# Kernel optimization log

Measured on AMD Instinct MI355X. Metric: run time of the kernel, lower is better.

Reference implementation:

```python
import jax, jax.numpy as jnp
import numpy as np

NUM_HEADS = 8


def setup_inputs() -> dict:
    key = jax.random.key(0)
    ks = jax.random.split(key, 10)
    B, C, H, W = 8, 256, 128, 128
    x_c = jax.random.normal(ks[0], (B, C, H, W), dtype=jnp.float32)
    x_t = jax.random.normal(ks[1], (B, C, H, W), dtype=jnp.float32)
    std = 0.02
    Wq = jax.random.normal(ks[2], (C, C), dtype=jnp.float32) * std
    Wk = jax.random.normal(ks[3], (C, C), dtype=jnp.float32) * std
    Wv = jax.random.normal(ks[4], (C, C), dtype=jnp.float32) * std
    Wo = jax.random.normal(ks[5], (C, C), dtype=jnp.float32) * std
    bq = jnp.zeros((C,), jnp.float32)
    bk = jnp.zeros((C,), jnp.float32)
    bv = jnp.zeros((C,), jnp.float32)
    bo = jnp.zeros((C,), jnp.float32)
    return {"x_c": x_c, "x_t": x_t, "Wq": Wq, "bq": bq, "Wk": Wk, "bk": bk,
            "Wv": Wv, "bv": bv, "Wo": Wo, "bo": bo}


def reference(x_c, x_t, Wq, bq, Wk, bk, Wv, bv, Wo, bo):
    B, C, H, W = x_c.shape
    nh = NUM_HEADS
    hd = C // nh                       # head_dim = in_chans // num_heads
    scale = hd ** (-0.5)
    N = H * W

    # fuse_type == 'add'
    x = (x_c + x_t).transpose(0, 2, 3, 1)          # [B,H,W,C]

    # torch Linear: y = x @ W.T + b
    q = x @ Wq.T + bq
    k = x @ Wk.T + bk
    v = x @ Wv.T + bv

    # 'b h w (c head) -> b (h w) head c' : head is the INNER split factor
    def split_heads(t):
        return t.reshape(B, N, hd, nh).transpose(0, 1, 3, 2)  # [B,N,nh,hd]

    q, k, v = split_heads(q), split_heads(k), split_heads(v)

    # attention ACROSS heads per token: [B,N,nh,nh] (faithful to source)
    dot = jnp.einsum('bnhc,bngc->bnhg', q, k) * scale
    attn = jax.nn.softmax(dot, axis=-1)
    o = jnp.einsum('bnhg,bngc->bnhc', attn, v)     # [B,N,nh,hd]

    # 'b (h w) head c -> b h w (head c)' : head is the OUTER concat factor
    o = o.reshape(B, H, W, nh * hd)
    out = o @ Wo.T + bo                            # [B,H,W,C]
    return out.transpose(0, 3, 1, 2)               # [B,C,H,W]
```

## Files before the change

### kernel.cpp

```cpp
#include <hip/hip_runtime.h>
#include <hip/hip_bf16.h>


typedef unsigned short u16;
typedef __bf16 bf16x8 __attribute__((ext_vector_type(8)));
typedef float f32x4 __attribute__((ext_vector_type(4)));
typedef unsigned short u16x8 __attribute__((ext_vector_type(8)));
typedef unsigned short u16x4 __attribute__((ext_vector_type(4)));

constexpr int CH = 256;
constexpr int HWN = 16384;
constexpr int LDX = 264;
constexpr int LQ = 776;

constexpr size_t WS_WQKV = 0;
constexpr size_t WS_WO = 393216;
constexpr size_t WS_BIAS = 524288;
constexpr size_t WS_O = 528384;

__device__ __forceinline__ u16 f2bf(float f) {
    unsigned u = __builtin_bit_cast(unsigned, f);
    unsigned r = u + 0x7FFFu + ((u >> 16) & 1u);
    return (u16)(r >> 16);
}
__device__ __forceinline__ float bf2f(u16 u) {
    return __builtin_bit_cast(float, (unsigned)u << 16);
}

__global__ void prep_kernel(const float* __restrict__ Wq, const float* __restrict__ Wk,
                            const float* __restrict__ Wv, const float* __restrict__ Wo,
                            const float* __restrict__ bq, const float* __restrict__ bk,
                            const float* __restrict__ bv,
                            u16* __restrict__ Wqkv_b, u16* __restrict__ Wo_b,
                            float* __restrict__ bias_qkv) {
    const int i = blockIdx.x;
    const int c = threadIdx.x;
    const int j = i & 255;
    const int p = ((j & 31) << 3) + (j >> 5);
    const float* Wsrc = (i < 256) ? Wq : (i < 512 ? Wk : Wv);
    const float* bsrc = (i < 256) ? bq : (i < 512 ? bk : bv);
    Wqkv_b[i * 256 + c] = f2bf(Wsrc[p * 256 + c]);
    if (i < 256) Wo_b[i * 256 + c] = f2bf(Wo[i * 256 + c]);
    if (c == 0) bias_qkv[i] = bsrc[p];
}

__launch_bounds__(512, 2)
__global__ void qkv_attn_kernel(const float* __restrict__ x_c, const float* __restrict__ x_t,
                                const u16* __restrict__ Wqkv_b,
                                const float* __restrict__ bias_qkv,
                                u16* __restrict__ O_glob) {
    __shared__ u16 XT[64 * LDX];
    __shared__ u16 QKVT[64 * LQ];

    const int tid = threadIdx.x;
    const int lane = tid & 63;
    const int wave = tid >> 6;
    const long tok0 = (long)blockIdx.x * 64;
    const int b = (int)(tok0 >> 14);
    const int hw0 = (int)(tok0 & (HWN - 1));
    const float* __restrict__ xc = x_c + (size_t)b * CH * HWN + hw0;
    const float* __restrict__ xt = x_t + (size_t)b * CH * HWN + hw0;

    {
        const int ltk = tid & 15;
        const int cp = tid >> 4;
        for (int pass = 0; pass < 4; ++pass) {
            const int c0 = pass * 64 + cp * 2;
#pragma unroll
            for (int ts = 0; ts < 4; ++ts) {
                const int t = ts * 16 + ltk;
                const float a0 = xc[c0 * HWN + t] + xt[c0 * HWN + t];
                const float a1 = xc[(c0 + 1) * HWN + t] + xt[(c0 + 1) * HWN + t];
                const unsigned pk = (unsigned)f2bf(a0) | ((unsigned)f2bf(a1) << 16);
                *(unsigned*)&XT[t * LDX + c0] = pk;
            }
        }
    }
    __syncthreads();

    {
        const int l15 = lane & 15;
        const int l4 = lane >> 4;
        const int m_base = wave * 96;
        f32x4 acc[6][4];
#pragma unroll
        for (int i = 0; i < 6; ++i)
#pragma unroll
            for (int j = 0; j < 4; ++j) acc[i][j] = (f32x4){0.f, 0.f, 0.f, 0.f};

#pragma unroll
        for (int kk = 0; kk < 8; ++kk) {
            const int koff = kk * 32 + l4 * 8;
            bf16x8 bfr[4];
#pragma unroll
            for (int ct = 0; ct < 4; ++ct)
                bfr[ct] = __builtin_bit_cast(bf16x8,
                    *(const u16x8*)&XT[(ct * 16 + l15) * LDX + koff]);
#pragma unroll
            for (int mt = 0; mt < 6; ++mt) {
                const int arow = m_base + mt * 16 + l15;
                const bf16x8 afr = __builtin_bit_cast(bf16x8,
                    *(const u16x8*)&Wqkv_b[arow * 256 + koff]);
#pragma unroll
                for (int ct = 0; ct < 4; ++ct)
                    acc[mt][ct] = __builtin_amdgcn_mfma_f32_16x16x32_bf16(
                        afr, bfr[ct], acc[mt][ct], 0, 0, 0);
            }
        }
        #pragma unroll
        for (int mt = 0; mt < 6; ++mt) {
            const int i0 = m_base + mt * 16 + l4 * 4;
            const f32x4 bias = *(const f32x4*)&bias_qkv[i0];
#pragma unroll
            for (int ct = 0; ct < 4; ++ct) {
                const int t = ct * 16 + l15;
                u16x4 pk;
#pragma unroll
                for (int r = 0; r < 4; ++r) pk[r] = f2bf(acc[mt][ct][r] + bias[r]);
                *(u16x4*)&QKVT[t * LQ + i0] = pk;
            }
        }
    }
    __syncthreads();

    {
        const int t = tid >> 3;
        const int h = tid & 7;
        const u16* __restrict__ row = &QKVT[t * LQ];
        float q[32];
#pragma unroll
        for (int i = 0; i < 4; ++i) {
            const u16x8 v = *(const u16x8*)&row[h * 32 + i * 8];
#pragma unroll
            for (int e = 0; e < 8; ++e) q[i * 8 + e] = bf2f(v[e]);
        }
        float dot[8];
#pragma unroll
        for (int g = 0; g < 8; ++g) {
            float s = 0.f;
#pragma unroll
            for (int i = 0; i < 4; ++i) {
                const u16x8 v = *(const u16x8*)&row[256 + g * 32 + i * 8];
#pragma unroll
                for (int e = 0; e < 8; ++e) s += q[i * 8 + e] * bf2f(v[e]);
            }
            dot[g] = s * 0.17677669529663687f;
        }
        float m = dot[0];
#pragma unroll
        for (int g = 1; g < 8; ++g) m = fmaxf(m, dot[g]);
        float ssum = 0.f;
#pragma unroll
        for (int g = 0; g < 8; ++g) { dot[g] = __expf(dot[g] - m); ssum += dot[g]; }
        const float rinv = 1.f / ssum;
        float o[32];
#pragma unroll
        for (int i = 0; i < 32; ++i) o[i] = 0.f;
#pragma unroll
        for (int g = 0; g < 8; ++g) {
            const float w = dot[g] * rinv;
#pragma unroll
            for (int i = 0; i < 4; ++i) {
                const u16x8 v = *(const u16x8*)&row[512 + g * 32 + i * 8];
#pragma unroll
                for (int e = 0; e < 8; ++e) o[i * 8 + e] += w * bf2f(v[e]);
            }
        }
        u16* __restrict__ orow = O_glob + (size_t)(tok0 + t) * 256 + h * 32;
#pragma unroll
        for (int i = 0; i < 4; ++i) {
            u16x8 pk;
#pragma unroll
            for (int e = 0; e < 8; ++e) pk[e] = f2bf(o[i * 8 + e]);
            *(u16x8*)&orow[i * 8] = pk;
        }
    }
}

__launch_bounds__(256, 2)
__global__ void out_gemm_kernel(const u16* __restrict__ O_glob,
                                const u16* __restrict__ Wo_b,
                                const float* __restrict__ bo,
                                float* __restrict__ out) {
    __shared__ u16 OT[64 * LDX];
    const int tid = threadIdx.x;
    const int lane = tid & 63;
    const int wave = tid >> 6;
    const long tok0 = (long)blockIdx.x * 64;

#pragma unroll
    for (int i = 0; i < 8; ++i) {
        const int idx = tid + i * 256;
        const int r = idx >> 5, c8 = idx & 31;
        *(u16x8*)&OT[r * LDX + c8 * 8] =
            *(const u16x8*)&O_glob[(size_t)(tok0 + r) * 256 + c8 * 8];
    }
    __syncthreads();

    const int l15 = lane & 15;
    const int l4 = lane >> 4;
    const int m_base = wave * 64;
    f32x4 acc[4][4];
#pragma unroll
    for (int i = 0; i < 4; ++i)
#pragma unroll
        for (int j = 0; j < 4; ++j) acc[i][j] = (f32x4){0.f, 0.f, 0.f, 0.f};

#pragma unroll
    for (int kk = 0; kk < 8; ++kk) {
        const int koff = kk * 32 + l4 * 8;
        bf16x8 bfr[4];
#pragma unroll
        for (int ct = 0; ct < 4; ++ct)
            bfr[ct] = __builtin_bit_cast(bf16x8,
                *(const u16x8*)&OT[(ct * 16 + l15) * LDX + koff]);
#pragma unroll
        for (int mt = 0; mt < 4; ++mt) {
            const int arow = m_base + mt * 16 + l15;
            const bf16x8 afr = __builtin_bit_cast(bf16x8,
                *(const u16x8*)&Wo_b[arow * 256 + koff]);
#pragma unroll
            for (int ct = 0; ct < 4; ++ct)
                acc[mt][ct] = __builtin_amdgcn_mfma_f32_16x16x32_bf16(
                    afr, bfr[ct], acc[mt][ct], 0, 0, 0);
        }
    }

#pragma unroll
    for (int mt = 0; mt < 4; ++mt) {
        const int c0 = m_base + mt * 16 + l4 * 4;
        const f32x4 bias = *(const f32x4*)&bo[c0];
#pragma unroll
        for (int ct = 0; ct < 4; ++ct) {
            const long t = tok0 + ct * 16 + l15;
            const int bb = (int)(t >> 14);
            const int hw = (int)(t & (HWN - 1));
            float* __restrict__ op = out + (((size_t)bb * 256 + c0) << 14) + hw;
#pragma unroll
            for (int r = 0; r < 4; ++r)
                op[(size_t)r << 14] = acc[mt][ct][r] + bias[r];
        }
    }
}

extern "C" void kernel_launch(void* const* d_in, const int* in_sizes, int n_in,
                              void* d_out, int out_size, void* d_ws, size_t ws_size,
                              hipStream_t stream) {
    const float* x_c = (const float*)d_in[0];
    const float* x_t = (const float*)d_in[1];
    const float* Wq = (const float*)d_in[2];
    const float* bq = (const float*)d_in[3];
    const float* Wk = (const float*)d_in[4];
    const float* bk = (const float*)d_in[5];
    const float* Wv = (const float*)d_in[6];
    const float* bv = (const float*)d_in[7];
    const float* Wo = (const float*)d_in[8];
    const float* bo = (const float*)d_in[9];
    float* out = (float*)d_out;
    char* ws = (char*)d_ws;

    u16* Wqkv_b = (u16*)(ws + WS_WQKV);
    u16* Wo_b = (u16*)(ws + WS_WO);
    float* bias_qkv = (float*)(ws + WS_BIAS);
    u16* O_glob = (u16*)(ws + WS_O);

    prep_kernel<<<768, 256, 0, stream>>>(Wq, Wk, Wv, Wo, bq, bk, bv,
                                         Wqkv_b, Wo_b, bias_qkv);
    qkv_attn_kernel<<<2048, 512, 0, stream>>>(x_c, x_t, Wqkv_b, bias_qkv, O_glob);
    out_gemm_kernel<<<2048, 256, 0, stream>>>(O_glob, Wo_b, bo, out);
}
```

Baseline: 489.3 us.

## Fuse output projection into QKV-attention kernel with 32-token tiles

New measurement: 600.7 us. +22.8%, slower.

```diff
diff --git a/kernel.cpp b/kernel.cpp
--- a/kernel.cpp
+++ b/kernel.cpp
@@ -10,13 +10,14 @@
 
 constexpr int CH = 256;
 constexpr int HWN = 16384;
-constexpr int LDX = 264;
-constexpr int LQ = 776;
+constexpr int T = 32;
+constexpr int LDXe = 272;
+constexpr int LDOe = 280;
+constexpr int LQe  = 776;
 
 constexpr size_t WS_WQKV = 0;
-constexpr size_t WS_WO = 393216;
+constexpr size_t WS_WO   = 393216;
 constexpr size_t WS_BIAS = 524288;
-constexpr size_t WS_O = 528384;
 
 __device__ __forceinline__ u16 f2bf(float f) {
     unsigned u = __builtin_bit_cast(unsigned, f);
@@ -44,37 +45,41 @@
     if (c == 0) bias_qkv[i] = bsrc[p];
 }
 
-__launch_bounds__(512, 2)
-__global__ void qkv_attn_kernel(const float* __restrict__ x_c, const float* __restrict__ x_t,
-                                const u16* __restrict__ Wqkv_b,
-                                const float* __restrict__ bias_qkv,
-                                u16* __restrict__ O_glob) {
-    __shared__ u16 XT[64 * LDX];
-    __shared__ u16 QKVT[64 * LQ];
+__launch_bounds__(512, 4)
+__global__ void fused_kernel(const float* __restrict__ x_c, const float* __restrict__ x_t,
+                             const u16* __restrict__ Wqkv_b, const u16* __restrict__ Wo_b,
+                             const float* __restrict__ bias_qkv, const float* __restrict__ bo,
+                             float* __restrict__ out) {
+    __shared__ u16 XO[T * LDOe];
+    __shared__ u16 QKVT[T * LQe];
 
     const int tid = threadIdx.x;
     const int lane = tid & 63;
     const int wave = tid >> 6;
-    const long tok0 = (long)blockIdx.x * 64;
-    const int b = (int)(tok0 >> 14);
-    const int hw0 = (int)(tok0 & (HWN - 1));
+    const int tok0 = blockIdx.x * T;
+    const int b = tok0 >> 14;
+    const int hw0 = tok0 & (HWN - 1);
     const float* __restrict__ xc = x_c + (size_t)b * CH * HWN + hw0;
     const float* __restrict__ xt = x_t + (size_t)b * CH * HWN + hw0;
 
     {
-        const int ltk = tid & 15;
-        const int cp = tid >> 4;
-        for (int pass = 0; pass < 4; ++pass) {
-            const int c0 = pass * 64 + cp * 2;
-#pragma unroll
-            for (int ts = 0; ts < 4; ++ts) {
-                const int t = ts * 16 + ltk;
-                const float a0 = xc[c0 * HWN + t] + xt[c0 * HWN + t];
-                const float a1 = xc[(c0 + 1) * HWN + t] + xt[(c0 + 1) * HWN + t];
-                const unsigned pk = (unsigned)f2bf(a0) | ((unsigned)f2bf(a1) << 16);
-                *(unsigned*)&XT[t * LDX + c0] = pk;
-            }
-        }
+        const int t2 = (tid & 15) * 2;
+        const int c0 = (tid >> 4) * 8;
+        float2 va[8], vb[8];
+#pragma unroll
+        for (int j = 0; j < 8; ++j) {
+            const size_t off = (size_t)(c0 + j) * HWN + t2;
+            va[j] = *(const float2*)&xc[off];
+            vb[j] = *(const float2*)&xt[off];
+        }
+        u16x8 r0, r1;
+#pragma unroll
+        for (int j = 0; j < 8; ++j) {
+            r0[j] = f2bf(va[j].x + vb[j].x);
+            r1[j] = f2bf(va[j].y + vb[j].y);
+        }
+        *(u16x8*)&XO[t2 * LDXe + c0] = r0;
+        *(u16x8*)&XO[(t2 + 1) * LDXe + c0] = r1;
     }
     __syncthreads();
 
@@ -82,51 +87,50 @@
         const int l15 = lane & 15;
         const int l4 = lane >> 4;
         const int m_base = wave * 96;
-        f32x4 acc[6][4];
+        f32x4 acc[6][2];
 #pragma unroll
         for (int i = 0; i < 6; ++i)
 #pragma unroll
-            for (int j = 0; j < 4; ++j) acc[i][j] = (f32x4){0.f, 0.f, 0.f, 0.f};
+            for (int j = 0; j < 2; ++j) acc[i][j] = (f32x4){0.f, 0.f, 0.f, 0.f};
 
 #pragma unroll
         for (int kk = 0; kk < 8; ++kk) {
             const int koff = kk * 32 + l4 * 8;
-            bf16x8 bfr[4];
-#pragma unroll
-            for (int ct = 0; ct < 4; ++ct)
+            bf16x8 bfr[2];
+#pragma unroll
+            for (int ct = 0; ct < 2; ++ct)
                 bfr[ct] = __builtin_bit_cast(bf16x8,
-                    *(const u16x8*)&XT[(ct * 16 + l15) * LDX + koff]);
+                    *(const u16x8*)&XO[(ct * 16 + l15) * LDXe + koff]);
 #pragma unroll
             for (int mt = 0; mt < 6; ++mt) {
-                const int arow = m_base + mt * 16 + l15;
                 const bf16x8 afr = __builtin_bit_cast(bf16x8,
-                    *(const u16x8*)&Wqkv_b[arow * 256 + koff]);
-#pragma unroll
-                for (int ct = 0; ct < 4; ++ct)
+                    *(const u16x8*)&Wqkv_b[(m_base + mt * 16 + l15) * 256 + koff]);
+#pragma unroll
+                for (int ct = 0; ct < 2; ++ct)
                     acc[mt][ct] = __builtin_amdgcn_mfma_f32_16x16x32_bf16(
                         afr, bfr[ct], acc[mt][ct], 0, 0, 0);
             }
         }
-        #pragma unroll
+#pragma unroll
         for (int mt = 0; mt < 6; ++mt) {
             const int i0 = m_base + mt * 16 + l4 * 4;
             const f32x4 bias = *(const f32x4*)&bias_qkv[i0];
 #pragma unroll
-            for (int ct = 0; ct < 4; ++ct) {
+            for (int ct = 0; ct < 2; ++ct) {
                 const int t = ct * 16 + l15;
                 u16x4 pk;
 #pragma unroll
                 for (int r = 0; r < 4; ++r) pk[r] = f2bf(acc[mt][ct][r] + bias[r]);
-                *(u16x4*)&QKVT[t * LQ + i0] = pk;
+                *(u16x4*)&QKVT[t * LQe + i0] = pk;
             }
         }
     }
     __syncthreads();
 
-    {
+    if (tid < T * 8) {
         const int t = tid >> 3;
         const int h = tid & 7;
-        const u16* __restrict__ row = &QKVT[t * LQ];
+        const u16* __restrict__ row = &QKVT[t * LQe];
         float q[32];
 #pragma unroll
         for (int i = 0; i < 4; ++i) {
@@ -166,79 +170,56 @@
                 for (int e = 0; e < 8; ++e) o[i * 8 + e] += w * bf2f(v[e]);
             }
         }
-        u16* __restrict__ orow = O_glob + (size_t)(tok0 + t) * 256 + h * 32;
 #pragma unroll
         for (int i = 0; i < 4; ++i) {
             u16x8 pk;
 #pragma unroll
             for (int e = 0; e < 8; ++e) pk[e] = f2bf(o[i * 8 + e]);
-            *(u16x8*)&orow[i * 8] = pk;
-        }
-    }
-}
-
-__launch_bounds__(256, 2)
-__global__ void out_gemm_kernel(const u16* __restrict__ O_glob,
-                                const u16* __restrict__ Wo_b,
-                                const float* __restrict__ bo,
-                                float* __restrict__ out) {
-    __shared__ u16 OT[64 * LDX];
-    const int tid = threadIdx.x;
-    const int lane = tid & 63;
-    const int wave = tid >> 6;
-    const long tok0 = (long)blockIdx.x * 64;
-
-#pragma unroll
-    for (int i = 0; i < 8; ++i) {
-        const int idx = tid + i * 256;
-        const int r = idx >> 5, c8 = idx & 31;
-        *(u16x8*)&OT[r * LDX + c8 * 8] =
-            *(const u16x8*)&O_glob[(size_t)(tok0 + r) * 256 + c8 * 8];
+            *(u16x8*)&XO[t * LDOe + h * 32 + i * 8] = pk;
+        }
     }
     __syncthreads();
 
-    const int l15 = lane & 15;
-    const int l4 = lane >> 4;
-    const int m_base = wave * 64;
-    f32x4 acc[4][4];
-#pragma unroll
-    for (int i = 0; i < 4; ++i)
-#pragma unroll
-        for (int j = 0; j < 4; ++j) acc[i][j] = (f32x4){0.f, 0.f, 0.f, 0.f};
-
-#pragma unroll
-    for (int kk = 0; kk < 8; ++kk) {
-        const int koff = kk * 32 + l4 * 8;
-        bf16x8 bfr[4];
-#pragma unroll
-        for (int ct = 0; ct < 4; ++ct)
-            bfr[ct] = __builtin_bit_cast(bf16x8,
-                *(const u16x8*)&OT[(ct * 16 + l15) * LDX + koff]);
-#pragma unroll
-        for (int mt = 0; mt < 4; ++mt) {
-            const int arow = m_base + mt * 16 + l15;
-            const bf16x8 afr = __builtin_bit_cast(bf16x8,
-                *(const u16x8*)&Wo_b[arow * 256 + koff]);
-#pragma unroll
-            for (int ct = 0; ct < 4; ++ct)
-                acc[mt][ct] = __builtin_amdgcn_mfma_f32_16x16x32_bf16(
-                    afr, bfr[ct], acc[mt][ct], 0, 0, 0);
-        }
-    }
-
-#pragma unroll
-    for (int mt = 0; mt < 4; ++mt) {
-        const int c0 = m_base + mt * 16 + l4 * 4;
-        const f32x4 bias = *(const f32x4*)&bo[c0];
-#pragma unroll
-        for (int ct = 0; ct < 4; ++ct) {
-            const long t = tok0 + ct * 16 + l15;
-            const int bb = (int)(t >> 14);
-            const int hw = (int)(t & (HWN - 1));
-            float* __restrict__ op = out + (((size_t)bb * 256 + c0) << 14) + hw;
-#pragma unroll
-            for (int r = 0; r < 4; ++r)
-                op[(size_t)r << 14] = acc[mt][ct][r] + bias[r];
+    {
+        const int l15 = lane & 15;
+        const int l4 = lane >> 4;
+        const int m_base = wave * 32;
+        f32x4 acc[2][2];
+#pragma unroll
+        for (int i = 0; i < 2; ++i)
+#pragma unroll
+            for (int j = 0; j < 2; ++j) acc[i][j] = (f32x4){0.f, 0.f, 0.f, 0.f};
+
+#pragma unroll
+        for (int kk = 0; kk < 8; ++kk) {
+            const int koff = kk * 32 + l4 * 8;
+            bf16x8 bfr[2];
+#pragma unroll
+            for (int ct = 0; ct < 2; ++ct)
+                bfr[ct] = __builtin_bit_cast(bf16x8,
+                    *(const u16x8*)&XO[(ct * 16 + l15) * LDOe + koff]);
+#pragma unroll
+            for (int mt = 0; mt < 2; ++mt) {
+                const bf16x8 afr = __builtin_bit_cast(bf16x8,
+                    *(const u16x8*)&Wo_b[(m_base + mt * 16 + l15) * 256 + koff]);
+#pragma unroll
+                for (int ct = 0; ct < 2; ++ct)
+                    acc[mt][ct] = __builtin_amdgcn_mfma_f32_16x16x32_bf16(
+                        afr, bfr[ct], acc[mt][ct], 0, 0, 0);
+            }
+        }
+#pragma unroll
+        for (int mt = 0; mt < 2; ++mt) {
+            const int c0 = m_base + mt * 16 + l4 * 4;
+            const f32x4 bias = *(const f32x4*)&bo[c0];
+#pragma unroll
+            for (int ct = 0; ct < 2; ++ct) {
+                const int hw = hw0 + ct * 16 + l15;
+                float* __restrict__ op = out + (((size_t)b * 256 + c0) << 14) + hw;
+#pragma unroll
+                for (int r = 0; r < 4; ++r)
+                    op[(size_t)r << 14] = acc[mt][ct][r] + bias[r];
+            }
         }
     }
 }
@@ -262,10 +243,9 @@
     u16* Wqkv_b = (u16*)(ws + WS_WQKV);
     u16* Wo_b = (u16*)(ws + WS_WO);
     float* bias_qkv = (float*)(ws + WS_BIAS);
-    u16* O_glob = (u16*)(ws + WS_O);
 
     prep_kernel<<<768, 256, 0, stream>>>(Wq, Wk, Wv, Wo, bq, bk, bv,
                                          Wqkv_b, Wo_b, bias_qkv);
-    qkv_attn_kernel<<<2048, 512, 0, stream>>>(x_c, x_t, Wqkv_b, bias_qkv, O_glob);
-    out_gemm_kernel<<<2048, 256, 0, stream>>>(O_glob, Wo_b, bo, out);
-}
+    fused_kernel<<<(8 * HWN) / T, 512, 0, stream>>>(x_c, x_t, Wqkv_b, Wo_b,
+                                                    bias_qkv, bo, out);
+}
```
